# Kernel optimization log

Hardware: AMD Instinct MI355X
Metric: run time of the kernel (lower is better)

Reference implementation:

```python
import jax, jax.numpy as jnp
import numpy as np

GRID = 32
GBOUND = 0.5
GRID_MIN = -GBOUND + GBOUND / GRID  # as in point2voxel


def _voxel_index(points):
    # points: [B,N,3] -> linear voxel indices [B,N]
    vx = (points - GRID_MIN) * GRID / (2.0 * GBOUND)
    vx = jnp.round(jnp.clip(vx, 0.0, GRID - 1))
    lin = vx @ jnp.array([GRID * GRID, GRID, 1], dtype=vx.dtype)
    return lin.astype(jnp.int32)


def _distance_loss(points, cps, v):
    # points [B,N,3], cps [B,G^3,3], v [B,G^3]
    lin = _voxel_index(points)                               # [B,N]
    mask = 1.0 - jnp.take_along_axis(v, lin, axis=1)         # [B,N]
    idx3 = jnp.broadcast_to(lin[:, :, None], lin.shape + (3,))
    gathered = jnp.take_along_axis(cps, idx3, axis=1)        # [B,N,3]
    d = (points - gathered) * mask[:, :, None]
    n2 = jnp.sum(d * d, axis=2)
    norm = jnp.sqrt(jnp.maximum(n2, 1e-30))                  # safe L2 norm
    return jnp.mean(jnp.sum(norm, axis=1))


def _plane_point(p, plane):
    # p [B,N,3], plane [B,1,4] -> reflected points [B,N,3]
    length = 2.0 * (jnp.sum(p * plane[..., :3], axis=2, keepdims=True) + plane[..., 3:4])
    norm2 = jnp.sum(plane[..., :3] ** 2, axis=2, keepdims=True)
    return p - length * plane[..., :3] / (norm2 + 1e-8)


def _quat_mul(q1, q2):
    w1, x1, y1, z1 = q1[..., 0], q1[..., 1], q1[..., 2], q1[..., 3]
    w2, x2, y2, z2 = q2[..., 0], q2[..., 1], q2[..., 2], q2[..., 3]
    w = w1 * w2 - x1 * x2 - y1 * y2 - z1 * z2
    x = w1 * x2 + x1 * w2 + y1 * z2 - z1 * y2
    y = w1 * y2 - x1 * z2 + y1 * w2 + z1 * x2
    z = w1 * z2 + x1 * y2 - y1 * x2 + z1 * w2
    return jnp.stack([w, x, y, z], axis=-1)


def _rotate_point(p, q):
    # p [B,N,3], q [B,1,4]
    B, N, _ = p.shape
    pq = jnp.concatenate([jnp.zeros((B, N, 1), p.dtype), p], axis=-1)
    qc = q * jnp.array([1.0, -1.0, -1.0, -1.0], q.dtype)
    return _quat_mul(_quat_mul(q, pq), qc)[..., 1:]


def setup_inputs() -> dict:
    key = jax.random.key(0)
    k = jax.random.split(key, 5)
    S, B, N, G = 3, 512, 1000, 32
    return {
        "planes": jax.random.normal(k[0], (S, B, 4), dtype=jnp.float32),
        "quats": jax.random.normal(k[1], (S, B, 4), dtype=jnp.float32),
        "closestPoints": jax.random.normal(k[2], (B, G ** 3 * 3), dtype=jnp.float32),
        "surfaceSamples": jax.random.normal(k[3], (B, N, 3), dtype=jnp.float32),
        "volume": jax.random.uniform(k[4], (B, 1, G, G, G), dtype=jnp.float32),
    }


def reference(planes, quats, closestPoints, surfaceSamples, volume):
    B = volume.shape[0]
    v = volume.reshape(B, GRID ** 3)
    cps = closestPoints.reshape(B, -1, 3)

    def per_sym(plane, quat):
        pl = plane[:, None, :]  # [B,1,4]
        lp = _distance_loss(_plane_point(surfaceSamples, pl), cps, v)
        qt = quat[:, None, :]
        lq = _distance_loss(_rotate_point(surfaceSamples, qt), cps, v)
        return lp, lq

    lps, lqs = jax.vmap(per_sym)(planes, quats)  # vectorized over S symmetry elems
    # sum over S then / S == mean, matching the torch loop
    return jnp.mean(lps), jnp.mean(lqs)
```

## Files before the change

### kernel.cpp

```cpp
#include <hip/hip_runtime.h>
#include <math.h>


#define GRID_N   32
#define NGRID3   32768
#define GRID_MIN_F (-0.484375f)

__device__ __forceinline__ float point_loss(float x, float y, float z,
                                            const float* __restrict__ vol,
                                            const float* __restrict__ cp)
{
    float fx = fminf(fmaxf((x - GRID_MIN_F) * 32.0f, 0.0f), 31.0f);
    float fy = fminf(fmaxf((y - GRID_MIN_F) * 32.0f, 0.0f), 31.0f);
    float fz = fminf(fmaxf((z - GRID_MIN_F) * 32.0f, 0.0f), 31.0f);
    int ix = (int)rintf(fx);
    int iy = (int)rintf(fy);
    int iz = (int)rintf(fz);
    int lin = ix * 1024 + iy * 32 + iz;

    float m  = 1.0f - vol[lin];
    float dx = (x - cp[lin * 3 + 0]) * m;
    float dy = (y - cp[lin * 3 + 1]) * m;
    float dz = (z - cp[lin * 3 + 2]) * m;
    float n2 = dx * dx + dy * dy + dz * dz;
    return sqrtf(fmaxf(n2, 1e-30f));
}

__global__ __launch_bounds__(256) void symloss_kernel(
    const float* __restrict__ planes,
    const float* __restrict__ quats,
    const float* __restrict__ cps,
    const float* __restrict__ samples,
    const float* __restrict__ volume,
    float* __restrict__ out,
    int S, int B, int N)
{
    const int b = blockIdx.x;
    const int s = blockIdx.y;

    const float* __restrict__ sp  = samples + (size_t)b * N * 3;
    const float* __restrict__ vol = volume  + (size_t)b * NGRID3;
    const float* __restrict__ cp  = cps     + (size_t)b * NGRID3 * 3;

    const float4 pl = ((const float4*)planes)[(size_t)s * B + b];
    const float4 q  = ((const float4*)quats )[(size_t)s * B + b];

    const float n2pl    = pl.x * pl.x + pl.y * pl.y + pl.z * pl.z;
    const float inv_n2  = 1.0f / (n2pl + 1e-8f);

    const float qw = q.x, qx = q.y, qy = q.z, qz = q.w;
    const float w2mu = qw * qw - (qx * qx + qy * qy + qz * qz);

    float sum_p = 0.0f, sum_q = 0.0f;

    for (int n = threadIdx.x; n < N; n += blockDim.x) {
        const float px = sp[n * 3 + 0];
        const float py = sp[n * 3 + 1];
        const float pz = sp[n * 3 + 2];

        {
            float len = 2.0f * (px * pl.x + py * pl.y + pz * pl.z + pl.w);
            float f   = len * inv_n2;
            float ax  = px - f * pl.x;
            float ay  = py - f * pl.y;
            float az  = pz - f * pl.z;
            sum_p += point_loss(ax, ay, az, vol, cp);
        }

        {
            float udp = qx * px + qy * py + qz * pz;
            float cx  = qy * pz - qz * py;
            float cy  = qz * px - qx * pz;
            float cz  = qx * py - qy * px;
            float bx  = w2mu * px + 2.0f * udp * qx + 2.0f * qw * cx;
            float by  = w2mu * py + 2.0f * udp * qy + 2.0f * qw * cy;
            float bz  = w2mu * pz + 2.0f * udp * qz + 2.0f * qw * cz;
            sum_q += point_loss(bx, by, bz, vol, cp);
        }
    }

    for (int off = 32; off > 0; off >>= 1) {
        sum_p += __shfl_down(sum_p, off);
        sum_q += __shfl_down(sum_q, off);
    }

    __shared__ float red[8][2];
    const int lane = threadIdx.x & 63;
    const int wid  = threadIdx.x >> 6;
    if (lane == 0) { red[wid][0] = sum_p; red[wid][1] = sum_q; }
    __syncthreads();

    if (threadIdx.x == 0) {
        const int nwaves = (blockDim.x + 63) >> 6;
        float tp = 0.0f, tq = 0.0f;
        for (int w = 0; w < nwaves; ++w) { tp += red[w][0]; tq += red[w][1]; }
        const float scale = 1.0f / (float)(S * B);
        atomicAdd(&out[0], tp * scale);
        atomicAdd(&out[1], tq * scale);
    }
}

extern "C" void kernel_launch(void* const* d_in, const int* in_sizes, int n_in,
                              void* d_out, int out_size, void* d_ws, size_t ws_size,
                              hipStream_t stream)
{
    const float* planes  = (const float*)d_in[0];
    const float* quats   = (const float*)d_in[1];
    const float* cps     = (const float*)d_in[2];
    const float* samples = (const float*)d_in[3];
    const float* volume  = (const float*)d_in[4];
    float* out = (float*)d_out;

    const int B = in_sizes[4] / NGRID3;
    const int S = in_sizes[0] / (B * 4);
    const int N = in_sizes[3] / (B * 3);

    hipMemsetAsync(d_out, 0, 2 * sizeof(float), stream);

    dim3 grid(B, S);
    symloss_kernel<<<grid, 256, 0, stream>>>(planes, quats, cps, samples,
                                             volume, out, S, B, N);
}
```

Measured before the change: 325.4 us.

## Fuse all symmetry elements into one block per batch and stage samples in LDS

The S dimension moves from the grid into each block: one block per batch item now loops over all S planes and quaternions, with the count fixed by a template parameter. The block's surface samples are first copied into shared memory with float4 loads and reused across every symmetry element. This makes the gathers from the same volume and closest-point arrays for all S elements run in one block, which can improve cache locality, and it adds more independent gathers per thread for latency hiding. The cost is a grid that is S times smaller (B blocks), more registers per thread, and dynamic LDS use for the samples.

```diff
diff --git a/kernel.cpp b/kernel.cpp
--- a/kernel.cpp
+++ b/kernel.cpp
@@ -2,9 +2,9 @@
 #include <math.h>
 
 
-#define GRID_N   32
-#define NGRID3   32768
+#define NGRID3     32768
 #define GRID_MIN_F (-0.484375f)
+#define NTHREADS   256
 
 __device__ __forceinline__ float point_loss(float x, float y, float z,
                                             const float* __restrict__ vol,
@@ -13,69 +13,71 @@
     float fx = fminf(fmaxf((x - GRID_MIN_F) * 32.0f, 0.0f), 31.0f);
     float fy = fminf(fmaxf((y - GRID_MIN_F) * 32.0f, 0.0f), 31.0f);
     float fz = fminf(fmaxf((z - GRID_MIN_F) * 32.0f, 0.0f), 31.0f);
-    int ix = (int)rintf(fx);
-    int iy = (int)rintf(fy);
-    int iz = (int)rintf(fz);
-    int lin = ix * 1024 + iy * 32 + iz;
+    int lin = ((int)rintf(fx)) * 1024 + ((int)rintf(fy)) * 32 + (int)rintf(fz);
 
     float m  = 1.0f - vol[lin];
     float dx = (x - cp[lin * 3 + 0]) * m;
     float dy = (y - cp[lin * 3 + 1]) * m;
     float dz = (z - cp[lin * 3 + 2]) * m;
-    float n2 = dx * dx + dy * dy + dz * dz;
-    return sqrtf(fmaxf(n2, 1e-30f));
+    return sqrtf(fmaxf(dx * dx + dy * dy + dz * dz, 1e-30f));
 }
 
-__global__ __launch_bounds__(256) void symloss_kernel(
+template <int S>
+__global__ __launch_bounds__(NTHREADS) void symloss_fused(
     const float* __restrict__ planes,
     const float* __restrict__ quats,
     const float* __restrict__ cps,
     const float* __restrict__ samples,
     const float* __restrict__ volume,
     float* __restrict__ out,
-    int S, int B, int N)
+    int B, int N, float scale)
 {
     const int b = blockIdx.x;
-    const int s = blockIdx.y;
+    const float* __restrict__ vol = volume + (size_t)b * NGRID3;
+    const float* __restrict__ cp  = cps    + (size_t)b * NGRID3 * 3;
 
-    const float* __restrict__ sp  = samples + (size_t)b * N * 3;
-    const float* __restrict__ vol = volume  + (size_t)b * NGRID3;
-    const float* __restrict__ cp  = cps     + (size_t)b * NGRID3 * 3;
+    extern __shared__ float spts[];
+    {
+        const float* sp = samples + (size_t)b * N * 3;
+        const int n4 = (N * 3) / 4;
+        const float4* src = (const float4*)sp;
+        float4* dst = (float4*)spts;
+        for (int i = threadIdx.x; i < n4; i += NTHREADS) dst[i] = src[i];
+        for (int i = n4 * 4 + threadIdx.x; i < N * 3; i += NTHREADS) spts[i] = sp[i];
+    }
 
-    const float4 pl = ((const float4*)planes)[(size_t)s * B + b];
-    const float4 q  = ((const float4*)quats )[(size_t)s * B + b];
+    float plx[S], ply[S], plz[S], plw[S], inv_n2[S];
+    float qw[S], qx[S], qy[S], qz[S], w2mu[S];
+#pragma unroll
+    for (int s = 0; s < S; ++s) {
+        float4 pl = ((const float4*)planes)[(size_t)s * B + b];
+        float4 q  = ((const float4*)quats )[(size_t)s * B + b];
+        plx[s] = pl.x; ply[s] = pl.y; plz[s] = pl.z; plw[s] = pl.w;
+        inv_n2[s] = 1.0f / (pl.x * pl.x + pl.y * pl.y + pl.z * pl.z + 1e-8f);
+        qw[s] = q.x; qx[s] = q.y; qy[s] = q.z; qz[s] = q.w;
+        w2mu[s] = q.x * q.x - (q.y * q.y + q.z * q.z + q.w * q.w);
+    }
 
-    const float n2pl    = pl.x * pl.x + pl.y * pl.y + pl.z * pl.z;
-    const float inv_n2  = 1.0f / (n2pl + 1e-8f);
-
-    const float qw = q.x, qx = q.y, qy = q.z, qz = q.w;
-    const float w2mu = qw * qw - (qx * qx + qy * qy + qz * qz);
+    __syncthreads();
 
     float sum_p = 0.0f, sum_q = 0.0f;
+    for (int n = threadIdx.x; n < N; n += NTHREADS) {
+        const float px = spts[n * 3 + 0];
+        const float py = spts[n * 3 + 1];
+        const float pz = spts[n * 3 + 2];
+#pragma unroll
+        for (int s = 0; s < S; ++s) {
+            float f = 2.0f * (px * plx[s] + py * ply[s] + pz * plz[s] + plw[s]) * inv_n2[s];
+            sum_p += point_loss(px - f * plx[s], py - f * ply[s], pz - f * plz[s], vol, cp);
 
-    for (int n = threadIdx.x; n < N; n += blockDim.x) {
-        const float px = sp[n * 3 + 0];
-        const float py = sp[n * 3 + 1];
-        const float pz = sp[n * 3 + 2];
-
-        {
-            float len = 2.0f * (px * pl.x + py * pl.y + pz * pl.z + pl.w);
-            float f   = len * inv_n2;
-            float ax  = px - f * pl.x;
-            float ay  = py - f * pl.y;
-            float az  = pz - f * pl.z;
-            sum_p += point_loss(ax, ay, az, vol, cp);
-        }
-
-        {
-            float udp = qx * px + qy * py + qz * pz;
-            float cx  = qy * pz - qz * py;
-            float cy  = qz * px - qx * pz;
-            float cz  = qx * py - qy * px;
-            float bx  = w2mu * px + 2.0f * udp * qx + 2.0f * qw * cx;
-            float by  = w2mu * py + 2.0f * udp * qy + 2.0f * qw * cy;
-            float bz  = w2mu * pz + 2.0f * udp * qz + 2.0f * qw * cz;
-            sum_q += point_loss(bx, by, bz, vol, cp);
+            float udp = qx[s] * px + qy[s] * py + qz[s] * pz;
+            float cx  = qy[s] * pz - qz[s] * py;
+            float cy  = qz[s] * px - qx[s] * pz;
+            float cz  = qx[s] * py - qy[s] * px;
+            sum_q += point_loss(w2mu[s] * px + 2.0f * (udp * qx[s] + qw[s] * cx),
+                                w2mu[s] * py + 2.0f * (udp * qy[s] + qw[s] * cy),
+                                w2mu[s] * pz + 2.0f * (udp * qz[s] + qw[s] * cz),
+                                vol, cp);
         }
     }
 
@@ -83,18 +85,15 @@
         sum_p += __shfl_down(sum_p, off);
         sum_q += __shfl_down(sum_q, off);
     }
-
-    __shared__ float red[8][2];
+    __shared__ float red[NTHREADS / 64][2];
     const int lane = threadIdx.x & 63;
     const int wid  = threadIdx.x >> 6;
     if (lane == 0) { red[wid][0] = sum_p; red[wid][1] = sum_q; }
     __syncthreads();
 
     if (threadIdx.x == 0) {
-        const int nwaves = (blockDim.x + 63) >> 6;
         float tp = 0.0f, tq = 0.0f;
-        for (int w = 0; w < nwaves; ++w) { tp += red[w][0]; tq += red[w][1]; }
-        const float scale = 1.0f / (float)(S * B);
+        for (int w = 0; w < NTHREADS / 64; ++w) { tp += red[w][0]; tq += red[w][1]; }
         atomicAdd(&out[0], tp * scale);
         atomicAdd(&out[1], tq * scale);
     }
@@ -114,10 +113,21 @@
     const int B = in_sizes[4] / NGRID3;
     const int S = in_sizes[0] / (B * 4);
     const int N = in_sizes[3] / (B * 3);
+    const float scale = 1.0f / (float)(S * B);
+    const size_t lds = (size_t)N * 3 * sizeof(float);
 
     hipMemsetAsync(d_out, 0, 2 * sizeof(float), stream);
 
-    dim3 grid(B, S);
-    symloss_kernel<<<grid, 256, 0, stream>>>(planes, quats, cps, samples,
-                                             volume, out, S, B, N);
+    switch (S) {
+    case 1: symloss_fused<1><<<B, NTHREADS, lds, stream>>>(planes, quats, cps, samples, volume, out, B, N, scale); break;
+    case 2: symloss_fused<2><<<B, NTHREADS, lds, stream>>>(planes, quats, cps, samples, volume, out, B, N, scale); break;
+    case 3: symloss_fused<3><<<B, NTHREADS, lds, stream>>>(planes, quats, cps, samples, volume, out, B, N, scale); break;
+    case 4: symloss_fused<4><<<B, NTHREADS, lds, stream>>>(planes, quats, cps, samples, volume, out, B, N, scale); break;
+    default:
+        for (int s = 0; s < S; ++s)
+            symloss_fused<1><<<B, NTHREADS, lds, stream>>>(planes + (size_t)s * B * 4,
+                                                           quats  + (size_t)s * B * 4,
+                                                           cps, samples, volume, out, B, N, scale);
+        break;
+    }
 }
```

Measured after the change: 307.0 us. 5.6% less time.
